# Kernel tuning notes

Measured on AMD Instinct MI355X. Metric: run time of the kernel, lower is better.

The kernel has to match this reference:

```python
import jax, jax.numpy as jnp
import numpy as np

NUM_HEADS = 8
WINDOW = 3
LOCAL_LEN = WINDOW * WINDOW
SR_RATIO = 8


def _normalize(v, eps=1e-12):
    n = jnp.linalg.norm(v, axis=-1, keepdims=True)
    return v / jnp.maximum(n, eps)


def _layernorm(v, g, b, eps=1e-5):
    m = v.mean(-1, keepdims=True)
    var = ((v - m) ** 2).mean(-1, keepdims=True)
    return (v - m) / jnp.sqrt(var + eps) * g + b


def _unfold3(x, H, W):
    # x: [B, C, H, W] -> [B, C, 9, H*W]  (kernel 3, pad 1, stride 1; torch nn.Unfold layout)
    B, C = x.shape[0], x.shape[1]
    xp = jnp.pad(x, ((0, 0), (0, 0), (1, 1), (1, 1)))
    patches = jnp.stack([xp[:, :, di:di + H, dj:dj + W]
                         for di in range(WINDOW) for dj in range(WINDOW)], axis=2)
    return patches.reshape(B, C, LOCAL_LEN, H * W)


def _forward(x, relative_coords_table, seq_length_scale, q_w, q_b, kv_w, kv_b,
             temperature, query_embedding, sr_w, sr_b, norm_g, norm_b,
             cpb_fc1_w, cpb_fc1_b, cpb_fc2_w, cpb_fc2_b,
             rel_bias_local, learnable_tokens, learnable_bias,
             proj_w, proj_b, relative_pos_index, padding_mask, H, W):
    B, N, C = x.shape
    hd = C // NUM_HEADS
    pool_H, pool_W = H // SR_RATIO, W // SR_RATIO
    pool_len = pool_H * pool_W

    # ---- queries ----
    q = (x @ q_w.T + q_b).reshape(B, N, NUM_HEADS, hd).transpose(0, 2, 1, 3)  # [B,h,N,d]
    q_norm = _normalize(q)
    q_scaled = (q_norm + query_embedding) * jax.nn.softplus(temperature) * seq_length_scale

    # ---- local k/v via unfold ----
    kv = x @ kv_w.T + kv_b  # [B,N,2C]
    k_loc = _normalize(kv[..., :C].reshape(B, N, NUM_HEADS, hd)).reshape(B, N, C)
    kv_img = jnp.concatenate([k_loc, kv[..., C:]], -1).transpose(0, 2, 1).reshape(B, 2 * C, H, W)
    kv_unf = _unfold3(kv_img, H, W).reshape(B, 2 * NUM_HEADS, hd, LOCAL_LEN, N)
    kv_unf = kv_unf.transpose(0, 1, 4, 2, 3)  # [B,2h,N,d,9]
    k_local, v_local = kv_unf[:, :NUM_HEADS], kv_unf[:, NUM_HEADS:]

    attn_local = jnp.einsum('bhnd,bhndl->bhnl', q_scaled, k_local) + rel_bias_local[:, None, :]
    attn_local = jnp.where(padding_mask, -jnp.inf, attn_local)

    # ---- pooled global k/v ----
    x_img = x.transpose(0, 2, 1).reshape(B, C, H, W)
    x_sr = jax.nn.gelu(jnp.einsum('oc,bchw->bohw', sr_w, x_img) + sr_b[None, :, None, None],
                       approximate=False)
    x_pool = x_sr.reshape(B, C, pool_H, SR_RATIO, pool_W, SR_RATIO).mean((3, 5))
    x_pool = x_pool.reshape(B, C, pool_len).transpose(0, 2, 1)
    x_pool = _layernorm(x_pool, norm_g, norm_b)
    kv_p = (x_pool @ kv_w.T + kv_b).reshape(B, pool_len, 2 * NUM_HEADS, hd).transpose(0, 2, 1, 3)
    k_pool, v_pool = kv_p[:, :NUM_HEADS], kv_p[:, NUM_HEADS:]

    # ---- continuous relative position bias (extrapolation path) ----
    cpb = jax.nn.relu(relative_coords_table @ cpb_fc1_w.T + cpb_fc1_b) @ cpb_fc2_w.T + cpb_fc2_b  # [T,h]
    pool_bias = cpb[relative_pos_index].reshape(N, pool_len, NUM_HEADS).transpose(2, 0, 1)  # [h,N,P]

    attn_pool = jnp.einsum('bhnd,bhpd->bhnp', q_scaled, _normalize(k_pool)) + pool_bias

    attn = jax.nn.softmax(jnp.concatenate([attn_local, attn_pool], -1), axis=-1)
    a_loc, a_pool = attn[..., :LOCAL_LEN], attn[..., LOCAL_LEN:]

    lt = jnp.einsum('bhnd,hdl->bhnl', q_norm, learnable_tokens) + learnable_bias + a_loc
    x_local = jnp.einsum('bhnl,bhndl->bhnd', lt, v_local)
    x_p = jnp.einsum('bhnp,bhpd->bhnd', a_pool, v_pool)
    out = (x_local + x_p).transpose(0, 2, 1, 3).reshape(B, N, C)
    return out @ proj_w.T + proj_b


def setup_inputs() -> dict:
    key = jax.random.key(0)
    B, H, W, C = 4, 64, 64, 256
    N = H * W
    hd = C // NUM_HEADS
    pool_H, pool_W = H // SR_RATIO, W // SR_RATIO
    pool_len = pool_H * pool_W

    # padding mask + per-query valid window length (get_seqlen_and_mask)
    ii, jj = np.meshgrid(np.arange(H), np.arange(W), indexing='ij')
    cols = []
    for di in range(WINDOW):
        for dj in range(WINDOW):
            ni, nj = ii + di - 1, jj + dj - 1
            cols.append(((ni < 0) | (ni >= H) | (nj < 0) | (nj >= W)).reshape(-1))
    padding_mask = np.stack(cols, -1)  # [N, 9], True = outside image
    local_len = (~padding_mask).sum(-1, keepdims=True).astype(np.float32)
    seq_length_scale = np.log(local_len + pool_len)  # [N, 1]

    # get_relative_position_cpb((H,W), (pool_H,pool_W))
    axis_q = np.arange(H, dtype=np.float64)
    axis_k = axis_q.reshape(pool_H, SR_RATIO).mean(-1)
    kh, kw = np.meshgrid(axis_k, axis_k, indexing='ij')
    qh, qw = np.meshgrid(axis_q, axis_q, indexing='ij')
    rel_h = (qh.ravel()[:, None] - kh.ravel()[None, :]) / (H - 1) * 8
    rel_w = (qw.ravel()[:, None] - kw.ravel()[None, :]) / (W - 1) * 8
    rel = np.stack([rel_h, rel_w], -1).reshape(-1, 2)
    table, idx = np.unique(rel, axis=0, return_inverse=True)
    table = np.sign(table) * np.log2(np.abs(table) + 1.0) / np.log2(8.0)

    ks = jax.random.split(key, 12)

    def nrm(k, shape, std=0.02):
        return jax.random.normal(k, shape, jnp.float32) * std

    return {
        'x': jax.random.normal(ks[0], (B, N, C), jnp.float32),
        'relative_coords_table': jnp.asarray(table, jnp.float32),
        'seq_length_scale': jnp.asarray(seq_length_scale, jnp.float32),
        'q_w': nrm(ks[1], (C, C)), 'q_b': jnp.zeros((C,), jnp.float32),
        'kv_w': nrm(ks[2], (2 * C, C)), 'kv_b': jnp.zeros((2 * C,), jnp.float32),
        'temperature': jnp.full((NUM_HEADS, 1, 1), float(np.log(np.expm1(1.0 / 0.24))), jnp.float32),
        'query_embedding': nrm(ks[3], (NUM_HEADS, 1, hd)),
        'sr_w': nrm(ks[4], (C, C)), 'sr_b': jnp.zeros((C,), jnp.float32),
        'norm_g': jnp.ones((C,), jnp.float32), 'norm_b': jnp.zeros((C,), jnp.float32),
        'cpb_fc1_w': nrm(ks[5], (512, 2), 0.1), 'cpb_fc1_b': jnp.zeros((512,), jnp.float32),
        'cpb_fc2_w': nrm(ks[6], (NUM_HEADS, 512)), 'cpb_fc2_b': jnp.zeros((NUM_HEADS,), jnp.float32),
        'rel_bias_local': nrm(ks[7], (NUM_HEADS, LOCAL_LEN), 0.0004),
        'learnable_tokens': nrm(ks[8], (NUM_HEADS, hd, LOCAL_LEN)),
        'learnable_bias': jnp.zeros((NUM_HEADS, 1, LOCAL_LEN), jnp.float32),
        'proj_w': nrm(ks[9], (C, C)), 'proj_b': jnp.zeros((C,), jnp.float32),
        'relative_pos_index': jnp.asarray(idx, jnp.int32),
        'padding_mask': jnp.asarray(padding_mask),
        'H': H, 'W': W,
    }


def reference(x, relative_coords_table, seq_length_scale, q_w, q_b, kv_w, kv_b,
              temperature, query_embedding, sr_w, sr_b, norm_g, norm_b,
              cpb_fc1_w, cpb_fc1_b, cpb_fc2_w, cpb_fc2_b,
              rel_bias_local, learnable_tokens, learnable_bias,
              proj_w, proj_b, relative_pos_index, padding_mask, H, W):
    return _forward(x, relative_coords_table, seq_length_scale, q_w, q_b, kv_w, kv_b,
                    temperature, query_embedding, sr_w, sr_b, norm_g, norm_b,
                    cpb_fc1_w, cpb_fc1_b, cpb_fc2_w, cpb_fc2_b,
                    rel_bias_local, learnable_tokens, learnable_bias,
                    proj_w, proj_b, relative_pos_index, padding_mask, H, W)
```

## Files before the change

kernel.cpp:

```cpp
#include <hip/hip_runtime.h>
#include <math.h>


typedef unsigned short ushort_t;
typedef __attribute__((ext_vector_type(8))) _Float16 half8;
typedef __attribute__((ext_vector_type(2))) _Float16 half2_t;
typedef __attribute__((ext_vector_type(4))) float f32x4;

static __device__ __forceinline__ ushort_t f2h(float f) {
    _Float16 h = (_Float16)f;
    return *(ushort_t*)&h;
}

static __device__ __forceinline__ float fdot2f(half2_t a, half2_t b, float c) {
#if __has_builtin(__builtin_amdgcn_fdot2)
    return __builtin_amdgcn_fdot2(a, b, c, false);
#else
    return (float)a[0] * (float)b[0] + (float)a[1] * (float)b[1] + c;
#endif
}

template <int CTRL>
static __device__ __forceinline__ float dpp_addf(float x) {
    int v = __builtin_amdgcn_update_dpp(
        0, __builtin_bit_cast(int, x), CTRL, 0xF, 0xF, true);
    return x + __builtin_bit_cast(float, v);
}
static __device__ __forceinline__ float quad_sumf(float x) {
    return dpp_addf<0x4E>(dpp_addf<0xB1>(x));
}
static __device__ __forceinline__ float sum16f(float x) {
    return dpp_addf<0x128>(dpp_addf<0x124>(quad_sumf(x)));
}

#define GLOAD16(g, l)                                                        \
    __builtin_amdgcn_global_load_lds(                                        \
        (const __attribute__((address_space(1))) unsigned int*)(g),          \
        (__attribute__((address_space(3))) unsigned int*)(l), 16, 0, 0)

template <int TM, int TN>
__global__ __launch_bounds__(256) void mfma_hgemm(
    const ushort_t* __restrict__ Ag, const ushort_t* __restrict__ Bg,
    const float* __restrict__ bias, float* __restrict__ out0,
    ushort_t* __restrict__ qh_out, ushort_t* __restrict__ kvh,
    ushort_t* __restrict__ xsrh, int mode)
{
    const int K = 256;
    const int IM = TM / 32;
    const int JN = TN / 32;
    constexpr int LPS = TM / 64 + TN / 64;
    __shared__ ushort_t Ah[2][TM * 32];
    __shared__ ushort_t Bh[2][TN * 32];

    const int t = threadIdx.x;
    const int w = t >> 6;
    const int lane = t & 63;

    const int nwg = gridDim.x * gridDim.y;
    int wg = blockIdx.y * gridDim.x + blockIdx.x;
    wg = (wg & 7) * (nwg >> 3) + (wg >> 3);
    const int bm = (wg / gridDim.x) * TM;
    const int bn = (wg % gridDim.x) * TN;

    const int wm = (w >> 1) * (TM / 2);
    const int wn = (w & 1) * (TN / 2);

    f32x4 acc[IM][JN];
#pragma unroll
    for (int i = 0; i < IM; ++i)
#pragma unroll
        for (int j = 0; j < JN; ++j) acc[i][j] = f32x4{0.f, 0.f, 0.f, 0.f};

    const int lrow  = t >> 2;
    const int lk8sw = ((t & 3) ^ ((t >> 3) & 3)) * 8;

#define STAGE(bufi, k0s)                                                     \
    do {                                                                     \
        _Pragma("unroll")                                                    \
        for (int r = 0; r < TM / 64; ++r)                                    \
            GLOAD16(Ag + (size_t)(bm + r * 64 + lrow) * K + (k0s) + lk8sw,   \
                    &Ah[bufi][(unsigned)(r * 64 + w * 16) * 32]);            \
        _Pragma("unroll")                                                    \
        for (int r = 0; r < TN / 64; ++r)                                    \
            GLOAD16(Bg + (size_t)(bn + r * 64 + lrow) * K + (k0s) + lk8sw,   \
                    &Bh[bufi][(unsigned)(r * 64 + w * 16) * 32]);            \
    } while (0)

    const int fr   = lane & 15;
    const int sws8 = ((lane >> 4) ^ ((fr >> 1) & 3)) * 8;

#define COMPUTE(bufi)                                                        \
    do {                                                                     \
        half8 af[IM], bf[JN];                                                \
        _Pragma("unroll")                                                    \
        for (int i2 = 0; i2 < IM; ++i2)                                      \
            af[i2] = *(const half8*)&Ah[bufi][(unsigned)(wm + i2 * 16 + fr) * 32 + sws8]; \
        _Pragma("unroll")                                                    \
        for (int j2 = 0; j2 < JN; ++j2)                                      \
            bf[j2] = *(const half8*)&Bh[bufi][(unsigned)(wn + j2 * 16 + fr) * 32 + sws8]; \
        __builtin_amdgcn_s_setprio(1);                                       \
        _Pragma("unroll")                                                    \
        for (int i2 = 0; i2 < IM; ++i2)                                      \
            _Pragma("unroll")                                                \
            for (int j2 = 0; j2 < JN; ++j2)                                  \
                acc[i2][j2] = __builtin_amdgcn_mfma_f32_16x16x32_f16(        \
                    af[i2], bf[j2], acc[i2][j2], 0, 0, 0);                   \
        __builtin_amdgcn_s_setprio(0);                                       \
    } while (0)

    STAGE(0, 0);
    STAGE(1, 32);
    int buf = 0;
#pragma unroll
    for (int s = 0; s < K / 32 - 1; ++s) {
        asm volatile("s_waitcnt vmcnt(%0)" :: "n"(LPS) : "memory");
        __builtin_amdgcn_s_barrier();
        asm volatile("" ::: "memory");
        COMPUTE(buf);
        asm volatile("" ::: "memory");
        __builtin_amdgcn_s_barrier();
        asm volatile("" ::: "memory");
        if (s + 2 < K / 32) STAGE(buf, (s + 2) * 32);
        buf ^= 1;
    }
    asm volatile("s_waitcnt vmcnt(0)" ::: "memory");
    __builtin_amdgcn_s_barrier();
    asm volatile("" ::: "memory");
    COMPUTE(buf);
#undef COMPUTE
#undef STAGE

    const int q4 = (lane >> 4) * 4;
#pragma unroll
    for (int i = 0; i < IM; ++i) {
#pragma unroll
        for (int jp = 0; jp < JN / 2; ++jp) {
#pragma unroll
            for (int r = 0; r < 4; ++r) {
                const int row = bm + wm + i * 16 + q4 + r;
                const int col0 = bn + wn + jp * 32 + fr;
                const int col1 = col0 + 16;
                float v0 = acc[i][2 * jp][r] + bias[col0];
                float v1 = acc[i][2 * jp + 1][r] + bias[col1];
                if (mode == 0) {
                    if (col0 < 256) {
                        qh_out[(size_t)row * 256 + col0] = f2h(v0);
                        qh_out[(size_t)row * 256 + col1] = f2h(v1);
                    } else if (col0 < 512) {
                        const float ss = sum16f(v0 * v0 + v1 * v1);
                        const float invn = 1.0f / fmaxf(sqrtf(ss), 1e-12f);
                        kvh[(size_t)row * 512 + (col0 - 256)] = f2h(v0 * invn);
                        kvh[(size_t)row * 512 + (col1 - 256)] = f2h(v1 * invn);
                    } else if (col0 < 768) {
                        kvh[(size_t)row * 512 + (col0 - 256)] = f2h(v0);
                        kvh[(size_t)row * 512 + (col1 - 256)] = f2h(v1);
                    } else {
                        v0 = 0.5f * v0 * (1.0f + erff(v0 * 0.70710678118654752f));
                        v1 = 0.5f * v1 * (1.0f + erff(v1 * 0.70710678118654752f));
                        xsrh[(size_t)row * 256 + (col0 - 768)] = f2h(v0);
                        xsrh[(size_t)row * 256 + (col1 - 768)] = f2h(v1);
                    }
                } else if (mode == 2) {
                    if (col0 < 256) {
                        const float ss = sum16f(v0 * v0 + v1 * v1);
                        const float invn = 1.0f / fmaxf(sqrtf(ss), 1e-12f);
                        v0 *= invn; v1 *= invn;
                    }
                    kvh[(size_t)row * 512 + col0] = f2h(v0);
                    kvh[(size_t)row * 512 + col1] = f2h(v1);
                } else {
                    out0[(size_t)row * 256 + col0] = v0;
                    out0[(size_t)row * 256 + col1] = v1;
                }
            }
        }
    }
}

__global__ __launch_bounds__(256) void prep_cpb(
    const float4* __restrict__ x, ushort4* __restrict__ xh, int n4, int nprep,
    const float* __restrict__ qw, const float* __restrict__ kvw,
    const float* __restrict__ srw, const float* __restrict__ pw,
    const float* __restrict__ qb, const float* __restrict__ kvb,
    const float* __restrict__ srb,
    ushort_t* __restrict__ Wall, ushort_t* __restrict__ Pw,
    float* __restrict__ ball,
    const float* __restrict__ table, const float* __restrict__ w1,
    const float* __restrict__ b1, const float* __restrict__ w2,
    const float* __restrict__ b2, float* __restrict__ outc, int T)
{
    if (blockIdx.x >= nprep) {
        const int wv = threadIdx.x >> 6;
        const int lane = threadIdx.x & 63;
        const int row = (blockIdx.x - nprep) * 4 + wv;
        if (row >= T) return;
        const float t0 = table[(size_t)row * 2];
        const float t1 = table[(size_t)row * 2 + 1];
        const int base = lane * 8;

        const float4* w1p = (const float4*)(w1 + (size_t)base * 2);
        float4 wa = w1p[0], wb = w1p[1], wc = w1p[2], wd = w1p[3];
        float4 ba = *(const float4*)(b1 + base);
        float4 bb = *(const float4*)(b1 + base + 4);
        float h[8];
        h[0] = fmaxf(fmaf(t1, wa.y, fmaf(t0, wa.x, ba.x)), 0.f);
        h[1] = fmaxf(fmaf(t1, wa.w, fmaf(t0, wa.z, ba.y)), 0.f);
        h[2] = fmaxf(fmaf(t1, wb.y, fmaf(t0, wb.x, ba.z)), 0.f);
        h[3] = fmaxf(fmaf(t1, wb.w, fmaf(t0, wb.z, ba.w)), 0.f);
        h[4] = fmaxf(fmaf(t1, wc.y, fmaf(t0, wc.x, bb.x)), 0.f);
        h[5] = fmaxf(fmaf(t1, wc.w, fmaf(t0, wc.z, bb.y)), 0.f);
        h[6] = fmaxf(fmaf(t1, wd.y, fmaf(t0, wd.x, bb.z)), 0.f);
        h[7] = fmaxf(fmaf(t1, wd.w, fmaf(t0, wd.z, bb.w)), 0.f);

#pragma unroll
        for (int hh = 0; hh < 8; ++hh) {
            const float4* w2p = (const float4*)(w2 + (size_t)hh * 512 + base);
            float4 p0 = w2p[0], p1 = w2p[1];
            float s = h[0]*p0.x + h[1]*p0.y + h[2]*p0.z + h[3]*p0.w
                    + h[4]*p1.x + h[5]*p1.y + h[6]*p1.z + h[7]*p1.w;
#pragma unroll
            for (int off = 1; off <= 32; off <<= 1) s += __shfl_xor(s, off);
            if (lane == 0) outc[(size_t)row * 8 + hh] = s + b2[hh];
        }
        return;
    }

    int idx = blockIdx.x * 256 + threadIdx.x;
    if (idx < n4) {
        float4 v = x[idx];
        ushort4 h;
        h.x = f2h(v.x); h.y = f2h(v.y); h.z = f2h(v.z); h.w = f2h(v.w);
        xh[idx] = h;
    }
    if (idx < 262144) {
        int nn = idx >> 8, k = idx & 255;
        float a;
        if (nn < 256)      a = qw[nn * 256 + k];
        else if (nn < 768) a = kvw[(nn - 256) * 256 + k];
        else               a = srw[(nn - 768) * 256 + k];
        Wall[idx] = f2h(a);
    }
    if (idx < 65536) Pw[idx] = f2h(pw[idx]);
    if (idx < 1024) {
        float bv;
        if (idx < 256)      bv = qb[idx];
        else if (idx < 768) bv = kvb[idx - 256];
        else                bv = srb[idx - 768];
        ball[idx] = bv;
    }
}

__global__ __launch_bounds__(256) void pool_ln(
    const ushort_t* __restrict__ xsr, const float* __restrict__ g,
    const float* __restrict__ be, ushort_t* __restrict__ xpool, int Hh, int Ww)
{
    const int C = 256;
    const int Nn = Hh * Ww;
    int b = blockIdx.x >> 6;
    int pidx = blockIdx.x & 63;
    int ph = pidx >> 3, pw = pidx & 7;
    int tid = threadIdx.x;
    float s = 0.f;
    for (int si = 0; si < 8; ++si) {
        int i = ph * 8 + si;
        const ushort_t* rowp = xsr + ((size_t)b * Nn + (size_t)i * Ww + pw * 8) * C + tid;
#pragma unroll
        for (int sj = 0; sj < 8; ++sj)
            s += (float)(*(const _Float16*)&rowp[(size_t)sj * C]);
    }
    s *= (1.f / 64.f);
    __shared__ float red[256];
    red[tid] = s; __syncthreads();
    for (int st = 128; st; st >>= 1) { if (tid < st) red[tid] += red[tid + st]; __syncthreads(); }
    float mean = red[0] * (1.f / 256.f);
    __syncthreads();
    float dv = s - mean;
    red[tid] = dv * dv; __syncthreads();
    for (int st = 128; st; st >>= 1) { if (tid < st) red[tid] += red[tid + st]; __syncthreads(); }
    float var = red[0] * (1.f / 256.f);
    xpool[(size_t)blockIdx.x * C + tid] = f2h(dv * rsqrtf(var + 1e-5f) * g[tid] + be[tid]);
}

__global__ __launch_bounds__(256) void attn_v8(
    const ushort_t* __restrict__ qh_g,
    const ushort_t* __restrict__ kvh,
    const ushort_t* __restrict__ kvph,
    const int* __restrict__ rpi,
    const float* __restrict__ cpbB,
    const float* __restrict__ sls, const float* __restrict__ temp,
    const float* __restrict__ qe, const float* __restrict__ rbl,
    const float* __restrict__ ltok, const float* __restrict__ lbias,
    ushort_t* __restrict__ attno_hf)
{
    const int h = blockIdx.y, b = blockIdx.z;
    const int t = threadIdx.x;
    const int i = blockIdx.x;

    __shared__ half8 kp_s[64][4];
    __shared__ half8 vp_s[64][4];
    __shared__ ushort_t pb_s[64][66];
    __shared__ float lts[9][32];
    __shared__ float rbl_s[9], lb_s[9], qe_s[32];

    {
        const int p = t >> 2;
        const int g4s = t & 3;
        const ushort_t* gk = kvph + ((size_t)(b * 64 + p)) * 512 + h * 32 + g4s * 8;
        kp_s[p][g4s] = *(const half8*)gk;
        vp_s[p][g4s] = *(const half8*)(gk + 256);
        const int rbase = i * 4096;
        for (int u = t; u < 4096; u += 256) {
            const int idx = rpi[rbase + u];
            pb_s[u >> 6][u & 63] = f2h(cpbB[(size_t)idx * 8 + h]);
        }
        for (int u = t; u < 288; u += 256) lts[u % 9][u / 9] = ltok[h * 288 + u];
        if (t < 9)  { rbl_s[t] = rbl[h * 9 + t]; lb_s[t] = lbias[h * 9 + t]; }
        if (t >= 64 && t < 96) qe_s[t - 64] = qe[h * 32 + (t - 64)];
    }
    __syncthreads();

    const int w = t >> 6;
    const int lane = t & 63;
    const int qi = lane >> 2;
    const int g4 = lane & 3;
    const int co = g4 * 8;
    const int j = w * 16 + qi;
    const int n = i * 64 + j;
    const size_t gq = (size_t)b * 4096 + n;

    const float tm = temp[h];
    const float sp = (tm > 20.f) ? tm : log1pf(expf(tm));

    float qv[8];
    {
        const half8 q8 = *(const half8*)(qh_g + gq * 256 + h * 32 + co);
        float ss = 0.f;
#pragma unroll
        for (int d = 0; d < 8; ++d) { qv[d] = (float)q8[d]; ss += qv[d] * qv[d]; }
        ss = quad_sumf(ss);
        const float invn = 1.0f / fmaxf(sqrtf(ss), 1e-12f);
#pragma unroll
        for (int d = 0; d < 8; ++d) qv[d] *= invn;
    }

    float lt[9];
#pragma unroll
    for (int l = 0; l < 9; ++l) {
        float dl = 0.f;
        const float4* lw = (const float4*)&lts[l][co];
#pragma unroll
        for (int c4 = 0; c4 < 2; ++c4) {
            float4 w4 = lw[c4];
            dl += qv[4*c4+0]*w4.x + qv[4*c4+1]*w4.y + qv[4*c4+2]*w4.z + qv[4*c4+3]*w4.w;
        }
        dl = quad_sumf(dl);
        lt[l] = dl + lb_s[l];
    }

    const float scal = sp * sls[n];
    half2_t qh[4];
#pragma unroll
    for (int c = 0; c < 4; ++c) {
        float a = (qv[2*c+0] + qe_s[co + 2*c+0]) * scal;
        float bq = (qv[2*c+1] + qe_s[co + 2*c+1]) * scal;
        qh[c] = half2_t{(_Float16)a, (_Float16)bq};
    }

    float sl[9];
#pragma unroll
    for (int l = 0; l < 9; ++l) {
        const int di = l / 3 - 1, dj = l % 3 - 1;
        const int ii = i + di;
        const int jn = j + dj;
        const bool ok = (ii >= 0) && (ii < 64) && (jn >= 0) && (jn < 64);
        const int ic = max(min(ii, 63), 0);
        const int jc = max(min(jn, 63), 0);
        const half8 k8 = *(const half8*)(kvh + ((size_t)(b * 4096 + ic * 64 + jc)) * 512 + h * 32 + co);
        float dk = 0.f;
        dk = fdot2f(qh[0], __builtin_shufflevector(k8, k8, 0, 1), dk);
        dk = fdot2f(qh[1], __builtin_shufflevector(k8, k8, 2, 3), dk);
        dk = fdot2f(qh[2], __builtin_shufflevector(k8, k8, 4, 5), dk);
        dk = fdot2f(qh[3], __builtin_shufflevector(k8, k8, 6, 7), dk);
        dk = quad_sumf(dk);
        sl[l] = ok ? (dk + rbl_s[l]) : -INFINITY;
    }

    float m = sl[0];
#pragma unroll
    for (int l = 1; l < 9; ++l) m = fmaxf(m, sl[l]);

    half2_t oh[4];
#pragma unroll
    for (int c = 0; c < 4; ++c) oh[c] = half2_t{(_Float16)0.f, (_Float16)0.f};
    float Z = 0.f;

    for (int cch = 0; cch < 8; ++cch) {
        float s8[8];
        float pbv[8];
#pragma unroll
        for (int c = 0; c < 4; ++c) {
            const half2_t p2 = *(const half2_t*)&pb_s[j][cch * 8 + 2 * c];
            pbv[2*c]   = (float)p2[0];
            pbv[2*c+1] = (float)p2[1];
        }
#pragma unroll
        for (int k = 0; k < 8; ++k) {
            const int p = cch * 8 + k;
            const half8 k8 = kp_s[p][g4];
            float acc = 0.f;
            acc = fdot2f(qh[0], __builtin_shufflevector(k8, k8, 0, 1), acc);
            acc = fdot2f(qh[1], __builtin_shufflevector(k8, k8, 2, 3), acc);
            acc = fdot2f(qh[2], __builtin_shufflevector(k8, k8, 4, 5), acc);
            acc = fdot2f(qh[3], __builtin_shufflevector(k8, k8, 6, 7), acc);
            acc = quad_sumf(acc);
            s8[k] = acc + pbv[k];
        }
        float cmax = s8[0];
#pragma unroll
        for (int k = 1; k < 8; ++k) cmax = fmaxf(cmax, s8[k]);
        const float m_new = fmaxf(m, cmax);
        const float factor = __expf(m - m_new);
        Z *= factor;
        const _Float16 fh = (_Float16)factor;
        const half2_t f2 = half2_t{fh, fh};
#pragma unroll
        for (int c = 0; c < 4; ++c) oh[c] *= f2;
        m = m_new;
#pragma unroll
        for (int k = 0; k < 8; ++k) {
            const float a = __expf(s8[k] - m);
            Z += a;
            const _Float16 ah = (_Float16)a;
            const half2_t a2 = half2_t{ah, ah};
            const half8 v8 = vp_s[cch * 8 + k][g4];
            oh[0] = a2 * __builtin_shufflevector(v8, v8, 0, 1) + oh[0];
            oh[1] = a2 * __builtin_shufflevector(v8, v8, 2, 3) + oh[1];
            oh[2] = a2 * __builtin_shufflevector(v8, v8, 4, 5) + oh[2];
            oh[3] = a2 * __builtin_shufflevector(v8, v8, 6, 7) + oh[3];
        }
    }

#pragma unroll
    for (int l = 0; l < 9; ++l) { sl[l] = __expf(sl[l] - m); Z += sl[l]; }

#pragma unroll
    for (int l = 0; l < 9; ++l) {
        const int di = l / 3 - 1, dj = l % 3 - 1;
        const int ii = i + di;
        const int jn = j + dj;
        const bool ok = (ii >= 0) && (ii < 64) && (jn >= 0) && (jn < 64);
        const int ic = max(min(ii, 63), 0);
        const int jc = max(min(jn, 63), 0);
        const float coef = ok ? (sl[l] + lt[l] * Z) : 0.f;
        const half8 v8 = *(const half8*)(kvh + ((size_t)(b * 4096 + ic * 64 + jc)) * 512 + 256 + h * 32 + co);
        const _Float16 ch = (_Float16)coef;
        const half2_t c2 = half2_t{ch, ch};
        oh[0] = c2 * __builtin_shufflevector(v8, v8, 0, 1) + oh[0];
        oh[1] = c2 * __builtin_shufflevector(v8, v8, 2, 3) + oh[1];
        oh[2] = c2 * __builtin_shufflevector(v8, v8, 4, 5) + oh[2];
        oh[3] = c2 * __builtin_shufflevector(v8, v8, 6, 7) + oh[3];
    }

    const float invZ = 1.0f / Z;
    ushort4* outp = (ushort4*)(attno_hf + gq * 256 + h * 32 + co);
#pragma unroll
    for (int c4 = 0; c4 < 2; ++c4) {
        ushort4 u;
        u.x = f2h((float)oh[2*c4+0][0] * invZ);
        u.y = f2h((float)oh[2*c4+0][1] * invZ);
        u.z = f2h((float)oh[2*c4+1][0] * invZ);
        u.w = f2h((float)oh[2*c4+1][1] * invZ);
        outp[c4] = u;
    }
}

extern "C" void kernel_launch(void* const* d_in, const int* in_sizes, int n_in,
                              void* d_out, int out_size, void* d_ws, size_t ws_size,
                              hipStream_t stream)
{
    const float* x    = (const float*)d_in[0];
    const float* tbl  = (const float*)d_in[1];
    const float* sls  = (const float*)d_in[2];
    const float* q_w  = (const float*)d_in[3];
    const float* q_b  = (const float*)d_in[4];
    const float* kv_w = (const float*)d_in[5];
    const float* kv_b = (const float*)d_in[6];
    const float* temp = (const float*)d_in[7];
    const float* qe   = (const float*)d_in[8];
    const float* sr_w = (const float*)d_in[9];
    const float* sr_b = (const float*)d_in[10];
    const float* ng   = (const float*)d_in[11];
    const float* nb   = (const float*)d_in[12];
    const float* f1w  = (const float*)d_in[13];
    const float* f1b  = (const float*)d_in[14];
    const float* f2w  = (const float*)d_in[15];
    const float* f2b  = (const float*)d_in[16];
    const float* rbl  = (const float*)d_in[17];
    const float* ltok = (const float*)d_in[18];
    const float* lbias= (const float*)d_in[19];
    const float* pw   = (const float*)d_in[20];
    const float* pb   = (const float*)d_in[21];
    const int*   rpi  = (const int*)d_in[22];

    const int C = 256, Hh = 64, Ww = 64, Nn = Hh * Ww;
    const int B = in_sizes[0] / (Nn * C);
    const int T = in_sizes[1] / 2;
    const int M = B * Nn;

    float* ws = (float*)d_ws;
    size_t o = 0;
    ushort_t* qh    = (ushort_t*)(ws + o); o += (size_t)M * C / 2;
    ushort_t* kvh   = (ushort_t*)(ws + o); o += (size_t)M * C;
    ushort_t* xsrh  = (ushort_t*)(ws + o); o += (size_t)M * C / 2;
    ushort_t* xpoolh= (ushort_t*)(ws + o); o += (size_t)B * 64 * C / 2;
    ushort_t* kvph  = (ushort_t*)(ws + o); o += (size_t)B * 64 * C;
    float* cpbB  = ws + o; o += (size_t)T * 8;
    ushort_t* xh   = (ushort_t*)(ws + o); o += (size_t)M * C / 2;
    ushort_t* Wall = (ushort_t*)(ws + o); o += 1024 * 256 / 2;
    ushort_t* Pwh  = (ushort_t*)(ws + o); o += 256 * 256 / 2;
    float* ball = ws + o; o += 1024;
    ushort_t* attno_hf = xh;

    dim3 blk(256);
    const int n4x = M * C / 4;
    const int nprep = (n4x + 255) / 256;
    const int ncpb  = (T + 3) / 4;

    prep_cpb<<<nprep + ncpb, blk, 0, stream>>>(
        (const float4*)x, (ushort4*)xh, n4x,
        nprep, q_w, kv_w, sr_w, pw, q_b, kv_b, sr_b, Wall, Pwh, ball,
        tbl, f1w, f1b, f2w, f2b, cpbB, T);
    mfma_hgemm<128, 64><<<dim3(16, M / 128), blk, 0, stream>>>(
        xh, Wall, ball, nullptr, qh, kvh, xsrh, 0);
    pool_ln<<<B * 64, blk, 0, stream>>>(xsrh, ng, nb, xpoolh, Hh, Ww);
    mfma_hgemm<64, 64><<<dim3(8, (B * 64) / 64), blk, 0, stream>>>(
        xpoolh, Wall + 256 * 256, ball + 256, nullptr, nullptr, kvph, nullptr, 2);
    attn_v8<<<dim3(64, 8, B), blk, 0, stream>>>(
        qh, kvh, kvph, rpi, cpbB, sls, temp, qe, rbl, ltok, lbias, attno_hf);
    mfma_hgemm<64, 64><<<dim3(4, M / 64), blk, 0, stream>>>(
        attno_hf, Pwh, pb, (float*)d_out, nullptr, nullptr, nullptr, 1);
}
```

Measured before the change: 208.0 us.

## Store q/kv/attention outputs head-major and stage local KV rows into LDS

The QKV and pooled-KV GEMM epilogues now write outputs head-major (per head, per token, 32 or 64 contiguous halves), and the projection GEMM reads its A operand in that layout. The attention kernel uses global_load_lds to stage the three neighbouring image rows of local K/V and the pooled K/V for its head into swizzled LDS, replacing scattered strided global loads per 3x3 neighbour. The aim is contiguous, coalesced loads and reuse of neighbour rows across the block. The cost is larger shared memory per block, which may lower occupancy, and more complex indexing.

New measurement: 219.3 us. 1.05x slower.

```diff
diff --git a/kernel.cpp b/kernel.cpp
--- a/kernel.cpp
+++ b/kernel.cpp
@@ -38,12 +38,12 @@
         (const __attribute__((address_space(1))) unsigned int*)(g),          \
         (__attribute__((address_space(3))) unsigned int*)(l), 16, 0, 0)
 
-template <int TM, int TN>
+template <int TM, int TN, bool AHM>
 __global__ __launch_bounds__(256) void mfma_hgemm(
     const ushort_t* __restrict__ Ag, const ushort_t* __restrict__ Bg,
     const float* __restrict__ bias, float* __restrict__ out0,
     ushort_t* __restrict__ qh_out, ushort_t* __restrict__ kvh,
-    ushort_t* __restrict__ xsrh, int mode)
+    ushort_t* __restrict__ xsrh, int mode, int Arows)
 {
     const int K = 256;
     const int IM = TM / 32;
@@ -77,9 +77,12 @@
 #define STAGE(bufi, k0s)                                                     \
     do {                                                                     \
         _Pragma("unroll")                                                    \
-        for (int r = 0; r < TM / 64; ++r)                                    \
-            GLOAD16(Ag + (size_t)(bm + r * 64 + lrow) * K + (k0s) + lk8sw,   \
-                    &Ah[bufi][(unsigned)(r * 64 + w * 16) * 32]);            \
+        for (int r = 0; r < TM / 64; ++r) {                                  \
+            const ushort_t* srcA = AHM                                       \
+                ? Ag + ((size_t)((k0s) >> 5) * Arows + (bm + r * 64 + lrow)) * 32 + lk8sw \
+                : Ag + (size_t)(bm + r * 64 + lrow) * K + (k0s) + lk8sw;     \
+            GLOAD16(srcA, &Ah[bufi][(unsigned)(r * 64 + w * 16) * 32]);      \
+        }                                                                    \
         _Pragma("unroll")                                                    \
         for (int r = 0; r < TN / 64; ++r)                                    \
             GLOAD16(Bg + (size_t)(bn + r * 64 + lrow) * K + (k0s) + lk8sw,   \
@@ -144,16 +147,19 @@
                 float v1 = acc[i][2 * jp + 1][r] + bias[col1];
                 if (mode == 0) {
                     if (col0 < 256) {
-                        qh_out[(size_t)row * 256 + col0] = f2h(v0);
-                        qh_out[(size_t)row * 256 + col1] = f2h(v1);
+                        const size_t base = ((size_t)(col0 >> 5) * Arows + row) * 32;
+                        qh_out[base + fr]      = f2h(v0);
+                        qh_out[base + fr + 16] = f2h(v1);
                     } else if (col0 < 512) {
                         const float ss = sum16f(v0 * v0 + v1 * v1);
                         const float invn = 1.0f / fmaxf(sqrtf(ss), 1e-12f);
-                        kvh[(size_t)row * 512 + (col0 - 256)] = f2h(v0 * invn);
-                        kvh[(size_t)row * 512 + (col1 - 256)] = f2h(v1 * invn);
+                        const size_t base = ((size_t)((col0 - 256) >> 5) * Arows + row) * 64;
+                        kvh[base + fr]      = f2h(v0 * invn);
+                        kvh[base + fr + 16] = f2h(v1 * invn);
                     } else if (col0 < 768) {
-                        kvh[(size_t)row * 512 + (col0 - 256)] = f2h(v0);
-                        kvh[(size_t)row * 512 + (col1 - 256)] = f2h(v1);
+                        const size_t base = ((size_t)((col0 - 512) >> 5) * Arows + row) * 64 + 32;
+                        kvh[base + fr]      = f2h(v0);
+                        kvh[base + fr + 16] = f2h(v1);
                     } else {
                         v0 = 0.5f * v0 * (1.0f + erff(v0 * 0.70710678118654752f));
                         v1 = 0.5f * v1 * (1.0f + erff(v1 * 0.70710678118654752f));
@@ -164,10 +170,14 @@
                     if (col0 < 256) {
                         const float ss = sum16f(v0 * v0 + v1 * v1);
                         const float invn = 1.0f / fmaxf(sqrtf(ss), 1e-12f);
-                        v0 *= invn; v1 *= invn;
+                        const size_t base = ((size_t)(col0 >> 5) * Arows + row) * 64;
+                        kvh[base + fr]      = f2h(v0 * invn);
+                        kvh[base + fr + 16] = f2h(v1 * invn);
+                    } else {
+                        const size_t base = ((size_t)((col0 - 256) >> 5) * Arows + row) * 64 + 32;
+                        kvh[base + fr]      = f2h(v0);
+                        kvh[base + fr + 16] = f2h(v1);
                     }
-                    kvh[(size_t)row * 512 + col0] = f2h(v0);
-                    kvh[(size_t)row * 512 + col1] = f2h(v1);
                 } else {
                     out0[(size_t)row * 256 + col0] = v0;
                     out0[(size_t)row * 256 + col1] = v1;
@@ -281,7 +291,7 @@
     xpool[(size_t)blockIdx.x * C + tid] = f2h(dv * rsqrtf(var + 1e-5f) * g[tid] + be[tid]);
 }
 
-__global__ __launch_bounds__(256) void attn_v8(
+__global__ __launch_bounds__(256) void attn_v9(
     const ushort_t* __restrict__ qh_g,
     const ushort_t* __restrict__ kvh,
     const ushort_t* __restrict__ kvph,
@@ -290,24 +300,43 @@
     const float* __restrict__ sls, const float* __restrict__ temp,
     const float* __restrict__ qe, const float* __restrict__ rbl,
     const float* __restrict__ ltok, const float* __restrict__ lbias,
-    ushort_t* __restrict__ attno_hf)
+    ushort_t* __restrict__ attno,
+    int Mtot)
 {
     const int h = blockIdx.y, b = blockIdx.z;
     const int t = threadIdx.x;
     const int i = blockIdx.x;
-
-    __shared__ half8 kp_s[64][4];
-    __shared__ half8 vp_s[64][4];
+    const int w = t >> 6;
+    const int lane = t & 63;
+
+    __shared__ ushort_t kvloc[3 * 64 * 64];
+    __shared__ ushort_t kvp[64 * 64];
     __shared__ ushort_t pb_s[64][66];
     __shared__ float lts[9][32];
     __shared__ float rbl_s[9], lb_s[9], qe_s[32];
 
     {
-        const int p = t >> 2;
-        const int g4s = t & 3;
-        const ushort_t* gk = kvph + ((size_t)(b * 64 + p)) * 512 + h * 32 + g4s * 8;
-        kp_s[p][g4s] = *(const half8*)gk;
-        vp_s[p][g4s] = *(const half8*)(gk + 256);
+        const int lt8 = lane >> 3, ls = lane & 7;
+#pragma unroll
+        for (int it = 0; it < 6; ++it) {
+            const int u = it * 4 + w;
+            const int dr = u >> 3, kB = u & 7;
+            const int srcRow = min(max(i - 1 + dr, 0), 63);
+            const int tok = kB * 8 + lt8;
+            GLOAD16(kvh + ((size_t)h * Mtot + b * 4096 + srcRow * 64) * 64
+                        + (size_t)(tok * 8 + (ls ^ (tok & 7))) * 8,
+                    &kvloc[(size_t)(dr * 64 + kB * 8) * 64]);
+        }
+#pragma unroll
+        for (int it = 0; it < 2; ++it) {
+            const int u = it * 4 + w;
+            const int tok = u * 8 + lt8;
+            GLOAD16(kvph + ((size_t)h * 256 + b * 64) * 64
+                         + (size_t)(tok * 8 + (ls ^ (tok & 7))) * 8,
+                    &kvp[(size_t)(u * 8) * 64]);
+        }
+    }
+    {
         const int rbase = i * 4096;
         for (int u = t; u < 4096; u += 256) {
             const int idx = rpi[rbase + u];
@@ -319,8 +348,6 @@
     }
     __syncthreads();
 
-    const int w = t >> 6;
-    const int lane = t & 63;
     const int qi = lane >> 2;
     const int g4 = lane & 3;
     const int co = g4 * 8;
@@ -333,7 +360,7 @@
 
     float qv[8];
     {
-        const half8 q8 = *(const half8*)(qh_g + gq * 256 + h * 32 + co);
+        const half8 q8 = *(const half8*)(qh_g + ((size_t)h * Mtot + gq) * 32 + co);
         float ss = 0.f;
 #pragma unroll
         for (int d = 0; d < 8; ++d) { qv[d] = (float)q8[d]; ss += qv[d] * qv[d]; }
@@ -373,9 +400,10 @@
         const int ii = i + di;
         const int jn = j + dj;
         const bool ok = (ii >= 0) && (ii < 64) && (jn >= 0) && (jn < 64);
-        const int ic = max(min(ii, 63), 0);
-        const int jc = max(min(jn, 63), 0);
-        const half8 k8 = *(const half8*)(kvh + ((size_t)(b * 4096 + ic * 64 + jc)) * 512 + h * 32 + co);
+        const int dr = di + 1;
+        const int tokc = max(min(jn, 63), 0);
+        const half8 k8 = *(const half8*)
+            &kvloc[(size_t)((dr * 64 + tokc) * 8 + (g4 ^ (tokc & 7))) * 8];
         float dk = 0.f;
         dk = fdot2f(qh[0], __builtin_shufflevector(k8, k8, 0, 1), dk);
         dk = fdot2f(qh[1], __builtin_shufflevector(k8, k8, 2, 3), dk);
@@ -406,7 +434,8 @@
 #pragma unroll
         for (int k = 0; k < 8; ++k) {
             const int p = cch * 8 + k;
-            const half8 k8 = kp_s[p][g4];
+            const half8 k8 = *(const half8*)
+                &kvp[(size_t)(p * 8 + (g4 ^ (p & 7))) * 8];
             float acc = 0.f;
             acc = fdot2f(qh[0], __builtin_shufflevector(k8, k8, 0, 1), acc);
             acc = fdot2f(qh[1], __builtin_shufflevector(k8, k8, 2, 3), acc);
@@ -430,9 +459,11 @@
         for (int k = 0; k < 8; ++k) {
             const float a = __expf(s8[k] - m);
             Z += a;
+            const int p = cch * 8 + k;
             const _Float16 ah = (_Float16)a;
             const half2_t a2 = half2_t{ah, ah};
-            const half8 v8 = vp_s[cch * 8 + k][g4];
+            const half8 v8 = *(const half8*)
+                &kvp[(size_t)(p * 8 + ((4 + g4) ^ (p & 7))) * 8];
             oh[0] = a2 * __builtin_shufflevector(v8, v8, 0, 1) + oh[0];
             oh[1] = a2 * __builtin_shufflevector(v8, v8, 2, 3) + oh[1];
             oh[2] = a2 * __builtin_shufflevector(v8, v8, 4, 5) + oh[2];
@@ -449,10 +480,11 @@
         const int ii = i + di;
         const int jn = j + dj;
         const bool ok = (ii >= 0) && (ii < 64) && (jn >= 0) && (jn < 64);
-        const int ic = max(min(ii, 63), 0);
-        const int jc = max(min(jn, 63), 0);
+        const int dr = di + 1;
+        const int tokc = max(min(jn, 63), 0);
         const float coef = ok ? (sl[l] + lt[l] * Z) : 0.f;
-        const half8 v8 = *(const half8*)(kvh + ((size_t)(b * 4096 + ic * 64 + jc)) * 512 + 256 + h * 32 + co);
+        const half8 v8 = *(const half8*)
+            &kvloc[(size_t)((dr * 64 + tokc) * 8 + ((4 + g4) ^ (tokc & 7))) * 8];
         const _Float16 ch = (_Float16)coef;
         const half2_t c2 = half2_t{ch, ch};
         oh[0] = c2 * __builtin_shufflevector(v8, v8, 0, 1) + oh[0];
@@ -462,7 +494,7 @@
     }
 
     const float invZ = 1.0f / Z;
-    ushort4* outp = (ushort4*)(attno_hf + gq * 256 + h * 32 + co);
+    ushort4* outp = (ushort4*)(attno + ((size_t)h * Mtot + gq) * 32 + co);
 #pragma unroll
     for (int c4 = 0; c4 < 2; ++c4) {
         ushort4 u;
@@ -530,13 +562,13 @@
         (const float4*)x, (ushort4*)xh, n4x,
         nprep, q_w, kv_w, sr_w, pw, q_b, kv_b, sr_b, Wall, Pwh, ball,
         tbl, f1w, f1b, f2w, f2b, cpbB, T);
-    mfma_hgemm<128, 64><<<dim3(16, M / 128), blk, 0, stream>>>(
-        xh, Wall, ball, nullptr, qh, kvh, xsrh, 0);
+    mfma_hgemm<128, 64, false><<<dim3(16, M / 128), blk, 0, stream>>>(
+        xh, Wall, ball, nullptr, qh, kvh, xsrh, 0, M);
     pool_ln<<<B * 64, blk, 0, stream>>>(xsrh, ng, nb, xpoolh, Hh, Ww);
-    mfma_hgemm<64, 64><<<dim3(8, (B * 64) / 64), blk, 0, stream>>>(
-        xpoolh, Wall + 256 * 256, ball + 256, nullptr, nullptr, kvph, nullptr, 2);
-    attn_v8<<<dim3(64, 8, B), blk, 0, stream>>>(
-        qh, kvh, kvph, rpi, cpbB, sls, temp, qe, rbl, ltok, lbias, attno_hf);
-    mfma_hgemm<64, 64><<<dim3(4, M / 64), blk, 0, stream>>>(
-        attno_hf, Pwh, pb, (float*)d_out, nullptr, nullptr, nullptr, 1);
-}
+    mfma_hgemm<64, 64, false><<<dim3(8, (B * 64) / 64), blk, 0, stream>>>(
+        xpoolh, Wall + 256 * 256, ball + 256, nullptr, nullptr, kvph, nullptr, 2, B * 64);
+    attn_v9<<<dim3(64, 8, B), blk, 0, stream>>>(
+        qh, kvh, kvph, rpi, cpbB, sls, temp, qe, rbl, ltok, lbias, attno_hf, M);
+    mfma_hgemm<64, 64, true><<<dim3(4, M / 64), blk, 0, stream>>>(
+        attno_hf, Pwh, pb, (float*)d_out, nullptr, nullptr, nullptr, 1, M);
+}
```
